# Kernel optimization log

Hardware: AMD Instinct MI355X
Metric: run time of the kernel (lower is better)

## Reference

```python
import jax, jax.numpy as jnp
import numpy as np

N_NODES = 100000
N_EDGES = 1600000
IN_CH = 128
HID = 64
HEADS = 2
OUT_CH = 2
EDGE_DIM = 3
NEG_SLOPE = 0.2
EPS = 1e-16  # PyG softmax denominator epsilon


def gat_conv(x, edge_index, edge_attr, W, We, att_src, att_dst, att_edge, bias, heads, out_ch, concat):
    """Faithful PyG GATConv (edge_dim enabled, eval mode, add_self_loops handled by caller=False here
    since the repo passes raw edge_index; PyG default add_self_loops=True is intentionally mirrored below)."""
    N = x.shape[0]
    src, dst = edge_index[0], edge_index[1]
    H, C = heads, out_ch
    h = (x @ W).reshape(N, H, C)                    # [N,H,C] node projections
    e = (edge_attr @ We).reshape(-1, H, C)          # [E,H,C] edge projections
    a_src = jnp.sum(h * att_src, axis=-1)           # [N,H]
    a_dst = jnp.sum(h * att_dst, axis=-1)           # [N,H]
    alpha = a_src[src] + a_dst[dst] + jnp.sum(e * att_edge, axis=-1)  # [E,H]
    alpha = jax.nn.leaky_relu(alpha, NEG_SLOPE)
    # segment softmax over incoming edges of each dst node
    amax = jax.ops.segment_max(alpha, dst, num_segments=N)            # [N,H]
    amax = jnp.where(jnp.isfinite(amax), amax, 0.0)
    alpha = jnp.exp(alpha - amax[dst])
    denom = jax.ops.segment_sum(alpha, dst, num_segments=N)           # [N,H]
    alpha = alpha / (denom[dst] + EPS)
    msg = h[src] * alpha[:, :, None]                                  # [E,H,C]
    out = jax.ops.segment_sum(msg, dst, num_segments=N)               # [N,H,C]
    if concat:
        out = out.reshape(N, H * C)
    else:
        out = out.mean(axis=1)
    return out + bias


def add_self_loops(edge_index, edge_attr, n):
    loops = jnp.arange(n, dtype=edge_index.dtype)
    ei = jnp.concatenate([edge_index, jnp.stack([loops, loops])], axis=1)
    ea = jnp.concatenate([edge_attr, jnp.zeros((n, edge_attr.shape[1]), edge_attr.dtype)], axis=0)
    return ei, ea


def setup_inputs() -> dict:
    key = jax.random.key(0)
    ks = jax.random.split(key, 16)
    s = 0.1
    x = jax.random.normal(ks[0], (N_NODES, IN_CH), jnp.float32)
    edge_index = jax.random.randint(ks[1], (2, N_EDGES), 0, N_NODES, jnp.int64 if jax.config.jax_enable_x64 else jnp.int32)
    edge_feat = jax.random.normal(ks[2], (N_EDGES, EDGE_DIM), jnp.float32)
    HC = HEADS * HID
    return {
        "x": x, "edge_index": edge_index, "edge_feat": edge_feat,
        "W1": jax.random.normal(ks[3], (IN_CH, HC), jnp.float32) * s,
        "We1": jax.random.normal(ks[4], (EDGE_DIM, HC), jnp.float32) * s,
        "as1": jax.random.normal(ks[5], (1, HEADS, HID), jnp.float32) * s,
        "ad1": jax.random.normal(ks[6], (1, HEADS, HID), jnp.float32) * s,
        "ae1": jax.random.normal(ks[7], (1, HEADS, HID), jnp.float32) * s,
        "b1": jnp.zeros((HC,), jnp.float32),
        "W2": jax.random.normal(ks[8], (HC, OUT_CH), jnp.float32) * s,
        "We2": jax.random.normal(ks[9], (EDGE_DIM, OUT_CH), jnp.float32) * s,
        "as2": jax.random.normal(ks[10], (1, 1, OUT_CH), jnp.float32) * s,
        "ad2": jax.random.normal(ks[11], (1, 1, OUT_CH), jnp.float32) * s,
        "ae2": jax.random.normal(ks[12], (1, 1, OUT_CH), jnp.float32) * s,
        "b2": jnp.zeros((OUT_CH,), jnp.float32),
    }


def reference(x, edge_index, edge_feat, W1, We1, as1, ad1, ae1, b1, W2, We2, as2, ad2, ae2, b2):
    # eval mode: F.dropout is identity
    ei, ea = add_self_loops(edge_index, edge_feat, x.shape[0])  # PyG GATConv default add_self_loops=True
    h = gat_conv(x, ei, ea, W1, We1, as1, ad1, ae1, b1, HEADS, HID, concat=True)
    h = jax.nn.elu(h)
    out = gat_conv(h, ei, ea, W2, We2, as2, ad2, ae2, b2, 1, OUT_CH, concat=False)
    return out
```

## Files before the change

kernel.cpp:

```cpp
#include <hip/hip_runtime.h>
#include <hip/hip_bf16.h>

#define NN 100000
#define NE 1600000
#define E2 (NE + NN)
#define NEG_SLOPE 0.2f
#define GEPS 1e-16f

typedef __attribute__((ext_vector_type(8))) short short8;
typedef __attribute__((ext_vector_type(4))) float f32x4;

__device__ __forceinline__ unsigned short f2b(float f) {
  unsigned u = __float_as_uint(f);
  u += 0x7fffu + ((u >> 16) & 1u);
  return (unsigned short)(u >> 16);
}
__device__ __forceinline__ float blo(unsigned u) { return __uint_as_float(u << 16); }
__device__ __forceinline__ float bhi(unsigned u) { return __uint_as_float(u & 0xffff0000u); }

__global__ void k_prep(const float* __restrict__ We1, const float* __restrict__ ae1,
                       const float* __restrict__ We2, const float* __restrict__ ae2,
                       const float* __restrict__ W1, const float* __restrict__ as1,
                       const float* __restrict__ ad1,
                       float* __restrict__ q, float4* __restrict__ pq) {
  int t = threadIdx.x;
  if (t < 6) {
    int d = t >> 1, hh = t & 1;
    float s = 0.f;
    for (int c = 0; c < 64; ++c) s += We1[d * 128 + hh * 64 + c] * ae1[hh * 64 + c];
    q[t] = s;
  } else if (t < 9) {
    int d = t - 6;
    q[8 + d] = We2[d * 2 + 0] * ae2[0] + We2[d * 2 + 1] * ae2[1];
  }
  if (t < 128) {
    float s0 = 0.f, s1 = 0.f, d0 = 0.f, d1 = 0.f;
    for (int c = 0; c < 64; ++c) {
      float w0 = W1[t * 128 + c], w1 = W1[t * 128 + 64 + c];
      s0 += w0 * as1[c];      s1 += w1 * as1[64 + c];
      d0 += w0 * ad1[c];      d1 += w1 * ad1[64 + c];
    }
    pq[t] = make_float4(s0, s1, d0, d1);
  }
}

__global__ __launch_bounds__(512, 4) void k_gemm(const float* __restrict__ x,
                                                 const float* __restrict__ W,
                                                 const float4* __restrict__ pq,
                                                 unsigned short* __restrict__ h1b,
                                                 float* __restrict__ a1s,
                                                 float* __restrict__ a1d) {
  __shared__ unsigned short xa[128 * 128];
  __shared__ unsigned short wt[128 * 128];
  int t = threadIdx.x;
  int row0 = blockIdx.x * 128;

  {
    int kr = t >> 2, n0 = (t & 3) * 32;
    const float* wp = &W[kr * 128 + n0];
    int cb = kr >> 3, klo = kr & 7;
#pragma unroll
    for (int j = 0; j < 8; ++j) {
      float4 v = *(const float4*)&wp[j * 4];
      int n = n0 + j * 4;
      wt[(n + 0) * 128 + ((cb ^ ((n + 0) & 15)) * 8) + klo] = f2b(v.x);
      wt[(n + 1) * 128 + ((cb ^ ((n + 1) & 15)) * 8) + klo] = f2b(v.y);
      wt[(n + 2) * 128 + ((cb ^ ((n + 2) & 15)) * 8) + klo] = f2b(v.z);
      wt[(n + 3) * 128 + ((cb ^ ((n + 3) & 15)) * 8) + klo] = f2b(v.w);
    }
  }
  {
    int lrow = t >> 2, qq = t & 3;
    int grow = row0 + lrow; if (grow >= NN) grow = NN - 1;
    const float* xp = &x[(size_t)grow * 128 + qq * 32];
    const float4* pqp = &pq[qq * 32];
    float ps0 = 0.f, ps1 = 0.f, pd0 = 0.f, pd1 = 0.f;
    int sw = lrow & 15;
#pragma unroll
    for (int j = 0; j < 4; ++j) {
      float4 u = *(const float4*)&xp[j * 8];
      float4 v = *(const float4*)&xp[j * 8 + 4];
      float xs[8] = {u.x, u.y, u.z, u.w, v.x, v.y, v.z, v.w};
      short8 sv;
#pragma unroll
      for (int e = 0; e < 8; ++e) {
        float4 pv = pqp[j * 8 + e];
        ps0 += xs[e] * pv.x; ps1 += xs[e] * pv.y;
        pd0 += xs[e] * pv.z; pd1 += xs[e] * pv.w;
        sv[e] = (short)f2b(xs[e]);
      }
      int c = qq * 4 + j;
      *(short8*)&xa[lrow * 128 + ((c ^ sw) * 8)] = sv;
    }
    ps0 += __shfl_xor(ps0, 1); ps0 += __shfl_xor(ps0, 2);
    ps1 += __shfl_xor(ps1, 1); ps1 += __shfl_xor(ps1, 2);
    pd0 += __shfl_xor(pd0, 1); pd0 += __shfl_xor(pd0, 2);
    pd1 += __shfl_xor(pd1, 1); pd1 += __shfl_xor(pd1, 2);
    if (qq == 0) {
      *(float2*)&a1s[grow * 2] = make_float2(ps0, ps1);
      *(float2*)&a1d[grow * 2] = make_float2(pd0, pd1);
    }
  }
  __syncthreads();

  int lane = t & 63, w = t >> 6;
  int m = lane & 15, quad = lane >> 4;
  int wm = (w & 1) * 64, wn = (w >> 1) * 32;
  f32x4 acc[4][2];
#pragma unroll
  for (int mi = 0; mi < 4; ++mi)
#pragma unroll
    for (int ni = 0; ni < 2; ++ni) acc[mi][ni] = (f32x4)(0.f);

#pragma unroll
  for (int kk = 0; kk < 4; ++kk) {
    int c = kk * 4 + quad;
    int co = (c ^ m) * 8;
    short8 a[4], b[2];
#pragma unroll
    for (int mi = 0; mi < 4; ++mi)
      a[mi] = *(const short8*)&xa[(wm + mi * 16 + m) * 128 + co];
#pragma unroll
    for (int ni = 0; ni < 2; ++ni)
      b[ni] = *(const short8*)&wt[(wn + ni * 16 + m) * 128 + co];
#pragma unroll
    for (int mi = 0; mi < 4; ++mi)
#pragma unroll
      for (int ni = 0; ni < 2; ++ni)
        acc[mi][ni] = __builtin_amdgcn_mfma_f32_16x16x32_bf16(a[mi], b[ni], acc[mi][ni], 0, 0, 0);
  }
#pragma unroll
  for (int mi = 0; mi < 4; ++mi)
#pragma unroll
    for (int r = 0; r < 4; ++r) {
      int grow = row0 + wm + mi * 16 + quad * 4 + r;
      if (grow >= NN) grow = NN - 1;
#pragma unroll
      for (int ni = 0; ni < 2; ++ni)
        h1b[(size_t)grow * 128 + wn + ni * 16 + m] = f2b(acc[mi][ni][r]);
    }
}

__global__ void k_hist(const int* __restrict__ ei, int* __restrict__ deg,
                       int* __restrict__ rank) {
  int t4 = blockIdx.x * 256 + threadIdx.x;
  if (t4 >= NE / 4) return;
  int4 d = *(const int4*)&ei[NE + t4 * 4];
  int4 rk;
  rk.x = atomicAdd(&deg[d.x], 1);
  rk.y = atomicAdd(&deg[d.y], 1);
  rk.z = atomicAdd(&deg[d.z], 1);
  rk.w = atomicAdd(&deg[d.w], 1);
  *(int4*)&rank[t4 * 4] = rk;
}

__global__ void k_scan1(const int* __restrict__ deg, int* __restrict__ bsum) {
  __shared__ int lds[256];
  int t = threadIdx.x;
  int base = blockIdx.x * 1024 + t * 4;
  int s = 0;
  for (int j = 0; j < 4; ++j) { int i = base + j; s += (i < NN) ? (deg[i] + 1) : 0; }
  lds[t] = s; __syncthreads();
  for (int o = 128; o > 0; o >>= 1) { if (t < o) lds[t] += lds[t + o]; __syncthreads(); }
  if (t == 0) bsum[blockIdx.x] = lds[0];
}

__global__ void k_scan2(int* __restrict__ bsum, int nb) {
  __shared__ int lds[128];
  int t = threadIdx.x;
  int v = (t < nb) ? bsum[t] : 0;
  lds[t] = v; __syncthreads();
  for (int o = 1; o < 128; o <<= 1) {
    int u = (t >= o) ? lds[t - o] : 0;
    __syncthreads();
    lds[t] += u;
    __syncthreads();
  }
  if (t < nb) bsum[t] = lds[t] - v;
}

__global__ void k_scan3(const int* __restrict__ deg, const int* __restrict__ bbase,
                        const float* __restrict__ a1s, const float* __restrict__ a1d,
                        int* __restrict__ rowptr, float4* __restrict__ cpk) {
  __shared__ int lds[256];
  int t = threadIdx.x;
  int base = blockIdx.x * 1024 + t * 4;
  int v[4]; int s = 0;
  for (int j = 0; j < 4; ++j) { int i = base + j; v[j] = (i < NN) ? (deg[i] + 1) : 0; s += v[j]; }
  lds[t] = s; __syncthreads();
  for (int o = 1; o < 256; o <<= 1) {
    int u = (t >= o) ? lds[t - o] : 0;
    __syncthreads();
    lds[t] += u;
    __syncthreads();
  }
  int excl = lds[t] - s + bbase[blockIdx.x];
  for (int j = 0; j < 4; ++j) {
    int i = base + j;
    if (i <= NN) rowptr[i] = excl;
    if (i < NN) {
      float al0 = a1s[i * 2] + a1d[i * 2];
      float al1 = a1s[i * 2 + 1] + a1d[i * 2 + 1];
      al0 = al0 > 0.f ? al0 : NEG_SLOPE * al0;
      al1 = al1 > 0.f ? al1 : NEG_SLOPE * al1;
      float4 pk;
      pk.x = __expf(al0); pk.y = __expf(al1);
      pk.z = __int_as_float(i); pk.w = 0.f;
      cpk[excl] = pk;
    }
    excl += v[j];
  }
}

__global__ void k_scatter(const int* __restrict__ ei, const float* __restrict__ ef,
                          const float* __restrict__ a1s, const float* __restrict__ a1d,
                          const float* __restrict__ q, const int* __restrict__ rowptr,
                          const int* __restrict__ rank, float4* __restrict__ cpk) {
  int t4 = blockIdx.x * 256 + threadIdx.x;
  if (t4 >= NE / 4) return;
  int e0 = t4 * 4;
  int4 ss = *(const int4*)&ei[e0];
  int4 dd = *(const int4*)&ei[NE + e0];
  int4 rk = *(const int4*)&rank[e0];
  float4 fA = *(const float4*)&ef[e0 * 3];
  float4 fB = *(const float4*)&ef[e0 * 3 + 4];
  float4 fC = *(const float4*)&ef[e0 * 3 + 8];
  float f[4][3] = {{fA.x, fA.y, fA.z}, {fA.w, fB.x, fB.y},
                   {fB.z, fB.w, fC.x}, {fC.y, fC.z, fC.w}};
  int src[4] = {ss.x, ss.y, ss.z, ss.w};
  int dst[4] = {dd.x, dd.y, dd.z, dd.w};
  int rnk[4] = {rk.x, rk.y, rk.z, rk.w};
#pragma unroll
  for (int j = 0; j < 4; ++j) {
    float e0h = f[j][0] * q[0] + f[j][1] * q[2] + f[j][2] * q[4];
    float e1h = f[j][0] * q[1] + f[j][1] * q[3] + f[j][2] * q[5];
    float ez  = f[j][0] * q[8] + f[j][1] * q[9] + f[j][2] * q[10];
    float al0 = a1s[src[j] * 2] + a1d[dst[j] * 2] + e0h;
    float al1 = a1s[src[j] * 2 + 1] + a1d[dst[j] * 2 + 1] + e1h;
    al0 = al0 > 0.f ? al0 : NEG_SLOPE * al0;
    al1 = al1 > 0.f ? al1 : NEG_SLOPE * al1;
    int pos = rowptr[dst[j]] + 1 + rnk[j];
    float4 pk;
    pk.x = __expf(al0); pk.y = __expf(al1);
    pk.z = __int_as_float(src[j]); pk.w = ez;
    cpk[pos] = pk;
  }
}

__global__ __launch_bounds__(256) void k_agg1(const unsigned short* __restrict__ h1b,
                                              const int* __restrict__ rowptr,
                                              const float4* __restrict__ cpk,
                                              const float* __restrict__ b1,
                                              const float* __restrict__ W2,
                                              const float* __restrict__ as2,
                                              const float* __restrict__ ad2,
                                              float* __restrict__ h2,
                                              float* __restrict__ a2s, float* __restrict__ a2d) {
  int n = (int)((blockIdx.x * 256 + threadIdx.x) >> 6);
  int lane = threadIdx.x & 63;
  if (n >= NN) return;
  int s0 = rowptr[n], s1 = rowptr[n + 1];
  int g = lane >> 4;
  int lp = lane & 15;
  bool head1 = lp >= 8;
  int slast = s1 - 1;

  float acc[8];
#pragma unroll
  for (int j = 0; j < 8; ++j) acc[j] = 0.f;
  float den = 0.f;

  for (int i = s0; i < s1; i += 8) {
    int iA = i + g, iB = i + 4 + g;
    int cA = iA < slast ? iA : slast;
    int cB = iB < slast ? iB : slast;
    float4 pA = cpk[cA];
    float4 pB = cpk[cB];
    const uint4* rA = (const uint4*)(h1b + ((size_t)__float_as_int(pA.z) << 7)) + lp;
    const uint4* rB = (const uint4*)(h1b + ((size_t)__float_as_int(pB.z) << 7)) + lp;
    uint4 vA = *rA;
    uint4 vB = *rB;
    float eA = head1 ? pA.y : pA.x;
    float eB = head1 ? pB.y : pB.x;
    eA = (iA < s1) ? eA : 0.f;
    eB = (iB < s1) ? eB : 0.f;
    den += eA + eB;
    acc[0] += eA * blo(vA.x) + eB * blo(vB.x);
    acc[1] += eA * bhi(vA.x) + eB * bhi(vB.x);
    acc[2] += eA * blo(vA.y) + eB * blo(vB.y);
    acc[3] += eA * bhi(vA.y) + eB * bhi(vB.y);
    acc[4] += eA * blo(vA.z) + eB * blo(vB.z);
    acc[5] += eA * bhi(vA.z) + eB * bhi(vB.z);
    acc[6] += eA * blo(vA.w) + eB * blo(vB.w);
    acc[7] += eA * bhi(vA.w) + eB * bhi(vB.w);
  }
#pragma unroll
  for (int o = 16; o <= 32; o <<= 1) {
    den += __shfl_xor(den, o);
#pragma unroll
    for (int j = 0; j < 8; ++j) acc[j] += __shfl_xor(acc[j], o);
  }
  float4 bA = *(const float4*)&b1[lp * 8];
  float4 bB = *(const float4*)&b1[lp * 8 + 4];
  float bb[8] = {bA.x, bA.y, bA.z, bA.w, bB.x, bB.y, bB.z, bB.w};
  float inv = 1.f / (den + GEPS);
  float r[8];
#pragma unroll
  for (int j = 0; j < 8; ++j) {
    float v = acc[j] * inv + bb[j];
    r[j] = v > 0.f ? v : __expf(v) - 1.f;
  }
  float4 wA = *(const float4*)&W2[lp * 16];
  float4 wB = *(const float4*)&W2[lp * 16 + 4];
  float4 wC = *(const float4*)&W2[lp * 16 + 8];
  float4 wD = *(const float4*)&W2[lp * 16 + 12];
  float p20 = r[0] * wA.x + r[1] * wA.z + r[2] * wB.x + r[3] * wB.z
            + r[4] * wC.x + r[5] * wC.z + r[6] * wD.x + r[7] * wD.z;
  float p21 = r[0] * wA.y + r[1] * wA.w + r[2] * wB.y + r[3] * wB.w
            + r[4] * wC.y + r[5] * wC.w + r[6] * wD.y + r[7] * wD.w;
#pragma unroll
  for (int o = 1; o <= 8; o <<= 1) { p20 += __shfl_xor(p20, o); p21 += __shfl_xor(p21, o); }
  if (lane == 0) {
    h2[n * 2] = p20; h2[n * 2 + 1] = p21;
    a2s[n] = p20 * as2[0] + p21 * as2[1];
    a2d[n] = p20 * ad2[0] + p21 * ad2[1];
  }
}

__global__ __launch_bounds__(256) void k_agg2(const int* __restrict__ rowptr,
                                              const float4* __restrict__ cpk,
                                              const float* __restrict__ h2,
                                              const float* __restrict__ a2s,
                                              const float* __restrict__ a2d,
                                              const float* __restrict__ b2,
                                              float* __restrict__ out) {
  int n = (int)((blockIdx.x * 256 + threadIdx.x) >> 6);
  int lane = threadIdx.x & 63;
  if (n >= NN) return;
  int s0 = rowptr[n], s1 = rowptr[n + 1];
  float adn = a2d[n];
  const float2* h2v = (const float2*)h2;
  float den = 0.f, acc0 = 0.f, acc1 = 0.f;
  for (int i = s0 + lane; i < s1; i += 64) {
    float4 pk = cpk[i];
    int s = __float_as_int(pk.z);
    float v = a2s[s] + adn + pk.w;
    v = v > 0.f ? v : NEG_SLOPE * v;
    float p = __expf(v);
    float2 hv = h2v[s];
    den += p;
    acc0 += p * hv.x;
    acc1 += p * hv.y;
  }
  for (int o = 32; o > 0; o >>= 1) {
    den += __shfl_xor(den, o);
    acc0 += __shfl_xor(acc0, o);
    acc1 += __shfl_xor(acc1, o);
  }
  if (lane == 0) {
    out[n * 2] = acc0 / (den + GEPS) + b2[0];
    out[n * 2 + 1] = acc1 / (den + GEPS) + b2[1];
  }
}

extern "C" void kernel_launch(void* const* d_in, const int* in_sizes, int n_in,
                              void* d_out, int out_size, void* d_ws, size_t ws_size,
                              hipStream_t stream) {
  (void)in_sizes; (void)n_in; (void)out_size; (void)ws_size;
  const float* x   = (const float*)d_in[0];
  const int*   ei  = (const int*)d_in[1];
  const float* ef  = (const float*)d_in[2];
  const float* W1  = (const float*)d_in[3];
  const float* We1 = (const float*)d_in[4];
  const float* as1 = (const float*)d_in[5];
  const float* ad1 = (const float*)d_in[6];
  const float* ae1 = (const float*)d_in[7];
  const float* b1  = (const float*)d_in[8];
  const float* W2  = (const float*)d_in[9];
  const float* We2 = (const float*)d_in[10];
  const float* as2 = (const float*)d_in[11];
  const float* ad2 = (const float*)d_in[12];
  const float* ae2 = (const float*)d_in[13];
  const float* b2  = (const float*)d_in[14];
  float* out = (float*)d_out;

  char* w = (char*)d_ws;
  auto alloc = [&](size_t bytes) -> char* {
    char* p = w; w += (bytes + 255) & ~(size_t)255; return p;
  };
  unsigned short* h1b = (unsigned short*)alloc((size_t)NN * 128 * 2);
  float*  a1s    = (float*)alloc((size_t)NN * 2 * 4);
  float*  a1d    = (float*)alloc((size_t)NN * 2 * 4);
  float*  h2     = (float*)alloc((size_t)NN * 2 * 4);
  float*  a2s    = (float*)alloc((size_t)NN * 4);
  float*  a2d    = (float*)alloc((size_t)NN * 4);
  float*  q      = (float*)alloc(64);
  float4* pq     = (float4*)alloc(128 * 16);
  int*    deg    = (int*)alloc((size_t)NN * 4);
  int*    rowptr = (int*)alloc((size_t)(NN + 1) * 4);
  int*    rank   = (int*)alloc((size_t)NE * 4);
  int*    bsum   = (int*)alloc(128 * 4);
  float4* cpk    = (float4*)alloc((size_t)E2 * 16);

  const int NB_SCAN = (NN + 1023) / 1024;

  hipLaunchKernelGGL(k_prep, dim3(1), dim3(128), 0, stream,
                     We1, ae1, We2, ae2, W1, as1, ad1, q, pq);
  hipLaunchKernelGGL(k_gemm, dim3((NN + 127) / 128), dim3(512), 0, stream,
                     x, W1, pq, h1b, a1s, a1d);
  hipMemsetAsync(deg, 0, (size_t)NN * 4, stream);
  hipLaunchKernelGGL(k_hist, dim3((NE / 4 + 255) / 256), dim3(256), 0, stream, ei, deg, rank);
  hipLaunchKernelGGL(k_scan1, dim3(NB_SCAN), dim3(256), 0, stream, deg, bsum);
  hipLaunchKernelGGL(k_scan2, dim3(1), dim3(128), 0, stream, bsum, NB_SCAN);
  hipLaunchKernelGGL(k_scan3, dim3(NB_SCAN), dim3(256), 0, stream,
                     deg, bsum, a1s, a1d, rowptr, cpk);
  hipLaunchKernelGGL(k_scatter, dim3((NE / 4 + 255) / 256), dim3(256), 0, stream,
                     ei, ef, a1s, a1d, q, rowptr, rank, cpk);
  hipLaunchKernelGGL(k_agg1, dim3((NN * 64 + 255) / 256), dim3(256), 0, stream,
                     h1b, rowptr, cpk, b1, W2, as2, ad2, h2, a2s, a2d);
  hipLaunchKernelGGL(k_agg2, dim3((NN * 64 + 255) / 256), dim3(256), 0, stream,
                     rowptr, cpk, h2, a2s, a2d, b2, out);
}
```

Measured before the change: 401.1 us.

## Pad CSR rows to multiples of eight, unroll agg1, pack node data, 4 nodes/wave in agg2

Each CSR row is padded to a multiple of 8 with zero-weight entries (pw=-1e30 so layer 2 exp gives zero), so agg1 can drop bounds clamps and masks and use a 16-edge unrolled loop. Layer-2 per-node values (h2, a2s, a2d) are packed into one float4 array, so each gather is a single load. agg2 now processes four nodes per wavefront with 16 lanes each, which suits the average degree of about 17. Padding adds extra cpk memory and writes in scan3, plus wasted gathers on padded slots.

```diff
diff --git a/kernel.cpp b/kernel.cpp
--- a/kernel.cpp
+++ b/kernel.cpp
@@ -3,7 +3,6 @@
 
 #define NN 100000
 #define NE 1600000
-#define E2 (NE + NN)
 #define NEG_SLOPE 0.2f
 #define GEPS 1e-16f
 
@@ -154,12 +153,14 @@
   *(int4*)&rank[t4 * 4] = rk;
 }
 
+__device__ __forceinline__ int padlen(int d) { return (d + 8) & ~7; }
+
 __global__ void k_scan1(const int* __restrict__ deg, int* __restrict__ bsum) {
   __shared__ int lds[256];
   int t = threadIdx.x;
   int base = blockIdx.x * 1024 + t * 4;
   int s = 0;
-  for (int j = 0; j < 4; ++j) { int i = base + j; s += (i < NN) ? (deg[i] + 1) : 0; }
+  for (int j = 0; j < 4; ++j) { int i = base + j; s += (i < NN) ? padlen(deg[i]) : 0; }
   lds[t] = s; __syncthreads();
   for (int o = 128; o > 0; o >>= 1) { if (t < o) lds[t] += lds[t + o]; __syncthreads(); }
   if (t == 0) bsum[blockIdx.x] = lds[0];
@@ -186,7 +187,7 @@
   int t = threadIdx.x;
   int base = blockIdx.x * 1024 + t * 4;
   int v[4]; int s = 0;
-  for (int j = 0; j < 4; ++j) { int i = base + j; v[j] = (i < NN) ? (deg[i] + 1) : 0; s += v[j]; }
+  for (int j = 0; j < 4; ++j) { int i = base + j; v[j] = (i < NN) ? padlen(deg[i]) : 0; s += v[j]; }
   lds[t] = s; __syncthreads();
   for (int o = 1; o < 256; o <<= 1) {
     int u = (t >= o) ? lds[t - o] : 0;
@@ -207,6 +208,9 @@
       pk.x = __expf(al0); pk.y = __expf(al1);
       pk.z = __int_as_float(i); pk.w = 0.f;
       cpk[excl] = pk;
+      float4 pad;
+      pad.x = 0.f; pad.y = 0.f; pad.z = __int_as_float(i); pad.w = -1e30f;
+      for (int k = 1 + deg[i]; k < v[j]; ++k) cpk[excl + k] = pad;
     }
     excl += v[j];
   }
@@ -254,8 +258,7 @@
                                               const float* __restrict__ W2,
                                               const float* __restrict__ as2,
                                               const float* __restrict__ ad2,
-                                              float* __restrict__ h2,
-                                              float* __restrict__ a2s, float* __restrict__ a2d) {
+                                              float4* __restrict__ nd) {
   int n = (int)((blockIdx.x * 256 + threadIdx.x) >> 6);
   int lane = threadIdx.x & 63;
   if (n >= NN) return;
@@ -263,27 +266,39 @@
   int g = lane >> 4;
   int lp = lane & 15;
   bool head1 = lp >= 8;
-  int slast = s1 - 1;
 
   float acc[8];
 #pragma unroll
   for (int j = 0; j < 8; ++j) acc[j] = 0.f;
   float den = 0.f;
 
-  for (int i = s0; i < s1; i += 8) {
-    int iA = i + g, iB = i + 4 + g;
-    int cA = iA < slast ? iA : slast;
-    int cB = iB < slast ? iB : slast;
-    float4 pA = cpk[cA];
-    float4 pB = cpk[cB];
-    const uint4* rA = (const uint4*)(h1b + ((size_t)__float_as_int(pA.z) << 7)) + lp;
-    const uint4* rB = (const uint4*)(h1b + ((size_t)__float_as_int(pB.z) << 7)) + lp;
-    uint4 vA = *rA;
-    uint4 vB = *rB;
+  int i = s0;
+  for (; i + 16 <= s1; i += 16) {
+    float4 pA = cpk[i + g], pB = cpk[i + 4 + g], pC = cpk[i + 8 + g], pD = cpk[i + 12 + g];
+    uint4 vA = *((const uint4*)(h1b + ((size_t)__float_as_int(pA.z) << 7)) + lp);
+    uint4 vB = *((const uint4*)(h1b + ((size_t)__float_as_int(pB.z) << 7)) + lp);
+    uint4 vC = *((const uint4*)(h1b + ((size_t)__float_as_int(pC.z) << 7)) + lp);
+    uint4 vD = *((const uint4*)(h1b + ((size_t)__float_as_int(pD.z) << 7)) + lp);
     float eA = head1 ? pA.y : pA.x;
     float eB = head1 ? pB.y : pB.x;
-    eA = (iA < s1) ? eA : 0.f;
-    eB = (iB < s1) ? eB : 0.f;
+    float eC = head1 ? pC.y : pC.x;
+    float eD = head1 ? pD.y : pD.x;
+    den += (eA + eB) + (eC + eD);
+    acc[0] += eA * blo(vA.x) + eB * blo(vB.x) + eC * blo(vC.x) + eD * blo(vD.x);
+    acc[1] += eA * bhi(vA.x) + eB * bhi(vB.x) + eC * bhi(vC.x) + eD * bhi(vD.x);
+    acc[2] += eA * blo(vA.y) + eB * blo(vB.y) + eC * blo(vC.y) + eD * blo(vD.y);
+    acc[3] += eA * bhi(vA.y) + eB * bhi(vB.y) + eC * bhi(vC.y) + eD * bhi(vD.y);
+    acc[4] += eA * blo(vA.z) + eB * blo(vB.z) + eC * blo(vC.z) + eD * blo(vD.z);
+    acc[5] += eA * bhi(vA.z) + eB * bhi(vB.z) + eC * bhi(vC.z) + eD * bhi(vD.z);
+    acc[6] += eA * blo(vA.w) + eB * blo(vB.w) + eC * blo(vC.w) + eD * blo(vD.w);
+    acc[7] += eA * bhi(vA.w) + eB * bhi(vB.w) + eC * bhi(vC.w) + eD * bhi(vD.w);
+  }
+  if (i < s1) {
+    float4 pA = cpk[i + g], pB = cpk[i + 4 + g];
+    uint4 vA = *((const uint4*)(h1b + ((size_t)__float_as_int(pA.z) << 7)) + lp);
+    uint4 vB = *((const uint4*)(h1b + ((size_t)__float_as_int(pB.z) << 7)) + lp);
+    float eA = head1 ? pA.y : pA.x;
+    float eB = head1 ? pB.y : pB.x;
     den += eA + eB;
     acc[0] += eA * blo(vA.x) + eB * blo(vB.x);
     acc[1] += eA * bhi(vA.x) + eB * bhi(vB.x);
@@ -321,45 +336,49 @@
 #pragma unroll
   for (int o = 1; o <= 8; o <<= 1) { p20 += __shfl_xor(p20, o); p21 += __shfl_xor(p21, o); }
   if (lane == 0) {
-    h2[n * 2] = p20; h2[n * 2 + 1] = p21;
-    a2s[n] = p20 * as2[0] + p21 * as2[1];
-    a2d[n] = p20 * ad2[0] + p21 * ad2[1];
+    float4 v;
+    v.x = p20; v.y = p21;
+    v.z = p20 * as2[0] + p21 * as2[1];
+    v.w = p20 * ad2[0] + p21 * ad2[1];
+    nd[n] = v;
   }
 }
 
 __global__ __launch_bounds__(256) void k_agg2(const int* __restrict__ rowptr,
                                               const float4* __restrict__ cpk,
-                                              const float* __restrict__ h2,
-                                              const float* __restrict__ a2s,
-                                              const float* __restrict__ a2d,
+                                              const float4* __restrict__ nd,
                                               const float* __restrict__ b2,
                                               float* __restrict__ out) {
-  int n = (int)((blockIdx.x * 256 + threadIdx.x) >> 6);
+  int wid = (int)((blockIdx.x * 256 + threadIdx.x) >> 6);
   int lane = threadIdx.x & 63;
+  int g = lane >> 4, lp = lane & 15;
+  int n = wid * 4 + g;
   if (n >= NN) return;
   int s0 = rowptr[n], s1 = rowptr[n + 1];
-  float adn = a2d[n];
-  const float2* h2v = (const float2*)h2;
+  float adn = nd[n].w;
   float den = 0.f, acc0 = 0.f, acc1 = 0.f;
-  for (int i = s0 + lane; i < s1; i += 64) {
+  for (int i = s0 + lp; i < s1; i += 16) {
     float4 pk = cpk[i];
     int s = __float_as_int(pk.z);
-    float v = a2s[s] + adn + pk.w;
+    float4 ns = nd[s];
+    float v = ns.z + adn + pk.w;
     v = v > 0.f ? v : NEG_SLOPE * v;
     float p = __expf(v);
-    float2 hv = h2v[s];
     den += p;
-    acc0 += p * hv.x;
-    acc1 += p * hv.y;
-  }
-  for (int o = 32; o > 0; o >>= 1) {
+    acc0 += p * ns.x;
+    acc1 += p * ns.y;
+  }
+#pragma unroll
+  for (int o = 1; o <= 8; o <<= 1) {
     den += __shfl_xor(den, o);
     acc0 += __shfl_xor(acc0, o);
     acc1 += __shfl_xor(acc1, o);
   }
-  if (lane == 0) {
-    out[n * 2] = acc0 / (den + GEPS) + b2[0];
-    out[n * 2 + 1] = acc1 / (den + GEPS) + b2[1];
+  if (lp == 0) {
+    float2 r;
+    r.x = acc0 / (den + GEPS) + b2[0];
+    r.y = acc1 / (den + GEPS) + b2[1];
+    *(float2*)&out[n * 2] = r;
   }
 }
 
@@ -391,16 +410,14 @@
   unsigned short* h1b = (unsigned short*)alloc((size_t)NN * 128 * 2);
   float*  a1s    = (float*)alloc((size_t)NN * 2 * 4);
   float*  a1d    = (float*)alloc((size_t)NN * 2 * 4);
-  float*  h2     = (float*)alloc((size_t)NN * 2 * 4);
-  float*  a2s    = (float*)alloc((size_t)NN * 4);
-  float*  a2d    = (float*)alloc((size_t)NN * 4);
+  float4* nd     = (float4*)alloc((size_t)NN * 16);
   float*  q      = (float*)alloc(64);
   float4* pq     = (float4*)alloc(128 * 16);
   int*    deg    = (int*)alloc((size_t)NN * 4);
   int*    rowptr = (int*)alloc((size_t)(NN + 1) * 4);
   int*    rank   = (int*)alloc((size_t)NE * 4);
   int*    bsum   = (int*)alloc(128 * 4);
-  float4* cpk    = (float4*)alloc((size_t)E2 * 16);
+  float4* cpk    = (float4*)alloc(((size_t)NE + 8 * NN) * 16);
 
   const int NB_SCAN = (NN + 1023) / 1024;
 
@@ -417,7 +434,7 @@
   hipLaunchKernelGGL(k_scatter, dim3((NE / 4 + 255) / 256), dim3(256), 0, stream,
                      ei, ef, a1s, a1d, q, rowptr, rank, cpk);
   hipLaunchKernelGGL(k_agg1, dim3((NN * 64 + 255) / 256), dim3(256), 0, stream,
-                     h1b, rowptr, cpk, b1, W2, as2, ad2, h2, a2s, a2d);
-  hipLaunchKernelGGL(k_agg2, dim3((NN * 64 + 255) / 256), dim3(256), 0, stream,
-                     rowptr, cpk, h2, a2s, a2d, b2, out);
-}
+                     h1b, rowptr, cpk, b1, W2, as2, ad2, nd);
+  hipLaunchKernelGGL(k_agg2, dim3(((NN + 3) / 4 * 64 + 255) / 256), dim3(256), 0, stream,
+                     rowptr, cpk, nd, b2, out);
+}
```

Result: faster. 388.1 us (-3.2%).
